# Kernel optimization log

Hardware: AMD Instinct MI355X
Metric: run time of the kernel (lower is better)

Reference implementation:

```python
import jax, jax.numpy as jnp
import numpy as np

T = 4096          # prefill tokens (single sequence)
HK = 16           # key heads
HV = 32           # value heads
DK = 128          # key head dim
DV = 128          # value head dim
K = 4             # causal conv kernel width
QKV = 2 * HK * DK + HV * DV  # 8192


def setup_inputs() -> dict:
    key = jax.random.key(0)
    k1, k2, k3, k4, k5, k6 = jax.random.split(key, 6)
    return {
        "mixed_qkv": jax.random.normal(k1, (T, QKV), dtype=jnp.float32),
        "a": jax.random.normal(k2, (T, HV), dtype=jnp.float32),
        "b": jax.random.normal(k3, (T, HV), dtype=jnp.float32),
        "conv_w": jax.random.normal(k4, (QKV, K), dtype=jnp.float32) * 0.2,
        "dt_bias": jax.random.normal(k5, (HV,), dtype=jnp.float32),
        "alog": jax.random.normal(k6, (HV,), dtype=jnp.float32),
    }


def _l2norm(x, eps=1e-6):
    return x * jax.lax.rsqrt(jnp.sum(x * x, axis=-1, keepdims=True) + eps)


def _forward(mixed_qkv, a, b, conv_w, dt_bias, alog):
    # --- causal depthwise conv1d (zero initial conv state) + SiLU ---
    xp = jnp.pad(mixed_qkv, ((K - 1, 0), (0, 0)))  # [T+K-1, QKV]
    y = sum(conv_w[None, :, j] * xp[j:j + T] for j in range(K))  # [T, QKV]
    x = jax.nn.silu(y)

    # --- split q/k/v ---
    q, k_, v = jnp.split(x, [HK * DK, 2 * HK * DK], axis=-1)
    q = q.reshape(T, HK, DK)
    k_ = k_.reshape(T, HK, DK)
    v = v.reshape(T, HV, DV)

    # use_qk_l2norm_in_kernel=True: L2-norm q,k; scale q by dk^-0.5
    q = _l2norm(q) * (DK ** -0.5)
    k_ = _l2norm(k_)

    # GQA: repeat key-head q/k to value-head count
    grp = HV // HK
    q = jnp.repeat(q, grp, axis=1)   # [T, HV, DK]
    k_ = jnp.repeat(k_, grp, axis=1)  # [T, HV, DK]

    # --- fused_gdn_gating ---
    g = -jnp.exp(alog)[None, :] * jax.nn.softplus(a + dt_bias[None, :])  # [T, HV]
    beta = jax.nn.sigmoid(b)                                             # [T, HV]

    # --- gated delta-rule recurrence (equiv. to chunk_gated_delta_rule) ---
    S0 = jnp.zeros((HV, DK, DV), dtype=mixed_qkv.dtype)

    def step(S, inp):
        qt, kt, vt, gt, bt = inp
        S = S * jnp.exp(gt)[:, None, None]                 # gated decay
        pred = jnp.einsum('hk,hkv->hv', kt, S)             # k^T S
        delta = (vt - pred) * bt[:, None]                  # beta-scaled error
        S = S + jnp.einsum('hk,hv->hkv', kt, delta)        # delta update
        o = jnp.einsum('hk,hkv->hv', qt, S)                # query readout
        return S, o

    _, out = jax.lax.scan(step, S0, (q, k_, v, g, beta))
    return out  # [T, HV, DV]


def reference(mixed_qkv, a, b, conv_w, dt_bias, alog):
    return _forward(mixed_qkv, a, b, conv_w, dt_bias, alog)
```

## Files before the change

kernel.cpp:

```cpp
#include <hip/hip_runtime.h>

#define T_LEN 4096
#define HKn   16
#define HVn   32
#define DKn   128
#define DVn   128
#define QKVn  8192
#define NCH   64
#define CS    64

typedef __attribute__((ext_vector_type(8))) short short8;
typedef __attribute__((ext_vector_type(4))) float f32x4;
typedef __attribute__((ext_vector_type(4))) unsigned u32x4;

#define OFF_QSH  ((size_t)0)
#define OFF_QSL  ((size_t)16777216)
#define OFF_KSH  ((size_t)33554432)
#define OFF_KSL  ((size_t)50331648)
#define OFF_KTH  ((size_t)67108864)
#define OFF_KTL  ((size_t)83886080)
#define OFF_VA   ((size_t)100663296)
#define OFF_GBL  ((size_t)167772160)
#define OFF_G    ((size_t)168820736)
#define OFF_WH   ((size_t)169345024)
#define OFF_WL   ((size_t)202899456)
#define OFF_MH   ((size_t)236453888)
#define OFF_ML   ((size_t)253231104)

template <int CTRL>
__device__ __forceinline__ float dpp_add(float x) {
    int v = __builtin_amdgcn_update_dpp(0, __float_as_int(x), CTRL, 0xF, 0xF, true);
    return x + __int_as_float(v);
}
__device__ __forceinline__ float reduce32g(float x) {
    x = dpp_add<0x128>(x); x = dpp_add<0x124>(x);
    x = dpp_add<0x122>(x); x = dpp_add<0x121>(x);
    int v = __builtin_amdgcn_ds_swizzle(__float_as_int(x), 0x401F);
    return x + __int_as_float(v);
}
__device__ __forceinline__ unsigned short bf16rne(float f) {
    unsigned x = __float_as_uint(f);
    return (unsigned short)((x + 0x7FFFu + ((x >> 16) & 1u)) >> 16);
}
__device__ __forceinline__ float bf16tof(unsigned short h) {
    return __uint_as_float(((unsigned)h) << 16);
}
__device__ __forceinline__ void bsplit(float f, unsigned short& h, unsigned short& l) {
    h = bf16rne(f);
    l = bf16rne(f - bf16tof(h));
}
__device__ __forceinline__ unsigned packsplit(float f) {
    unsigned short h, l; bsplit(f, h, l);
    return ((unsigned)h << 16) | (unsigned)l;
}
__device__ __forceinline__ f32x4 MF(short8 a, short8 b, f32x4 c) {
    return __builtin_amdgcn_mfma_f32_16x16x32_bf16(a, b, c, 0, 0, 0);
}
__device__ __forceinline__ void unpack8(u32x4 x0, u32x4 x1, short8& hi, short8& lo) {
    union { u32x4 u; short8 s; } H, L;
    H.u[0] = __builtin_amdgcn_perm(x0.y, x0.x, 0x07060302u);
    L.u[0] = __builtin_amdgcn_perm(x0.y, x0.x, 0x05040100u);
    H.u[1] = __builtin_amdgcn_perm(x0.w, x0.z, 0x07060302u);
    L.u[1] = __builtin_amdgcn_perm(x0.w, x0.z, 0x05040100u);
    H.u[2] = __builtin_amdgcn_perm(x1.y, x1.x, 0x07060302u);
    L.u[2] = __builtin_amdgcn_perm(x1.y, x1.x, 0x05040100u);
    H.u[3] = __builtin_amdgcn_perm(x1.w, x1.z, 0x07060302u);
    L.u[3] = __builtin_amdgcn_perm(x1.w, x1.z, 0x05040100u);
    hi = H.s; lo = L.s;
}
#define SB0() __builtin_amdgcn_sched_barrier(0)
#define BARL() do { \
    asm volatile("s_waitcnt lgkmcnt(0)" ::: "memory"); \
    __builtin_amdgcn_s_barrier(); \
    asm volatile("" ::: "memory"); \
} while (0)

__global__ __launch_bounds__(256) void k_gate(
    const float* __restrict__ a, const float* __restrict__ b,
    const float* __restrict__ dt_bias, const float* __restrict__ alog,
    float2* __restrict__ gbl)
{
    const int i = blockIdx.x * 256 + threadIdx.x;
    if (i < T_LEN * HVn) {
        const int h = i >> 12, t = i & (T_LEN - 1);
        const float av = a[(size_t)t * HVn + h];
        const float bv = b[(size_t)t * HVn + h];
        const float xv = av + dt_bias[h];
        const float sp = fmaxf(xv, 0.f) + log1pf(expf(-fabsf(xv)));
        const float g  = -expf(alog[h]) * sp;
        const float beta = 1.f / (1.f + expf(-bv));
        gbl[(size_t)h * T_LEN + t] = make_float2(beta, g);
    }
}

__global__ __launch_bounds__(128) void k_conv(
    const float* __restrict__ x, const float* __restrict__ w,
    const float* __restrict__ bgate,
    unsigned short* __restrict__ qsh, unsigned short* __restrict__ qsl,
    unsigned short* __restrict__ ksh, unsigned short* __restrict__ ksl,
    float* __restrict__ va2)
{
    const int t = blockIdx.x, seg = blockIdx.y, d = threadIdx.x;
    const int c = seg * 128 + d;
    const float4 w4 = ((const float4*)w)[c];
    float acc;
    if (t >= 3) {
        const float* xc = x + (size_t)(t - 3) * QKVn + c;
        acc = fmaf(w4.x, xc[0], fmaf(w4.y, xc[(size_t)QKVn],
              fmaf(w4.z, xc[(size_t)2 * QKVn], w4.w * xc[(size_t)3 * QKVn])));
    } else {
        float a0 = (t - 3 >= 0) ? x[(size_t)(t - 3) * QKVn + c] : 0.f;
        float a1 = (t - 2 >= 0) ? x[(size_t)(t - 2) * QKVn + c] : 0.f;
        float a2 = (t - 1 >= 0) ? x[(size_t)(t - 1) * QKVn + c] : 0.f;
        float a3 = x[(size_t)t * QKVn + c];
        acc = fmaf(w4.x, a0, fmaf(w4.y, a1, fmaf(w4.z, a2, w4.w * a3)));
    }
    const float y = acc / (1.f + expf(-acc));

    if (seg < 32) {
        float ss = reduce32g(y * y);
        __shared__ float part[4];
        if ((threadIdx.x & 31) == 0) part[threadIdx.x >> 5] = ss;
        __syncthreads();
        const float total = part[0] + part[1] + part[2] + part[3];
        const float r = rsqrtf(total + 1e-6f);
        float o = y * r;
        unsigned short hh, ll;
        if (seg < 16) {
            o *= 0.08838834764831845f;
            bsplit(o, hh, ll);
            const size_t idx = ((size_t)seg * T_LEN + t) * DKn + d;
            qsh[idx] = hh; qsl[idx] = ll;
        } else {
            bsplit(o, hh, ll);
            const size_t idx = ((size_t)(seg - 16) * T_LEN + t) * DKn + d;
            ksh[idx] = hh; ksl[idx] = ll;
        }
    } else {
        const int h = seg - 32;
        const float bv = bgate[(size_t)t * HVn + h];
        const float beta = 1.f / (1.f + expf(-bv));
        va2[((size_t)h * T_LEN + t) * DVn + d] = y * beta;
    }
}

__global__ __launch_bounds__(256) void k_tr(
    const unsigned short* __restrict__ ksh, const unsigned short* __restrict__ ksl,
    unsigned short* __restrict__ kth, unsigned short* __restrict__ ktl)
{
    __shared__ unsigned pk[64][65];
    const int b = blockIdx.x;
    const int kh = b >> 7, tt = (b >> 1) & 63, hh = b & 1;
    const int t0 = tt * 64, d0 = hh * 64;
    const int tid = threadIdx.x;
    #pragma unroll
    for (int e = 0; e < 16; ++e) {
        const int lin = e * 256 + tid;
        const int tl = lin >> 6, dl = lin & 63;
        const size_t o = ((size_t)kh * T_LEN + t0 + tl) * DKn + d0 + dl;
        pk[tl][dl] = ((unsigned)ksh[o] << 16) | (unsigned)ksl[o];
    }
    __syncthreads();
    #pragma unroll
    for (int e = 0; e < 16; ++e) {
        const int lin = e * 256 + tid;
        const int dl = lin >> 6, tl = lin & 63;
        const unsigned v = pk[tl][dl];
        const size_t o = ((size_t)kh * DKn + d0 + dl) * T_LEN + t0 + tl;
        kth[o] = (unsigned short)(v >> 16);
        ktl[o] = (unsigned short)(v & 0xFFFF);
    }
}

__global__ __launch_bounds__(256) void k_p1(
    const float2* __restrict__ gbl,
    const unsigned short* __restrict__ qsh, const unsigned short* __restrict__ qsl,
    const unsigned short* __restrict__ ksh, const unsigned short* __restrict__ ksl,
    float* __restrict__ va2, float* __restrict__ Gbuf,
    unsigned short* __restrict__ Wh, unsigned short* __restrict__ Wl,
    unsigned short* __restrict__ Mh, unsigned short* __restrict__ Ml)
{
    __shared__ float sA[64][68];
    __shared__ float sG[64];
    __shared__ float sB[64];
    const int blk = blockIdx.x;
    const int h = blk >> 6, ch = blk & 63;
    const int kh = h >> 1, t0 = ch * 64;
    const int tid = threadIdx.x, lane = tid & 63, wid = tid >> 6;
    const int l15 = lane & 15, lg = lane >> 4;

    if (tid < 64) {
        float2 g2 = gbl[(size_t)h * T_LEN + t0 + tid];
        sB[tid] = g2.x;
        float G = g2.y;
        #pragma unroll
        for (int s = 1; s < 64; s <<= 1) {
            float y = __int_as_float(__builtin_amdgcn_ds_bpermute((tid - s) << 2, __float_as_int(G)));
            G += (tid >= s) ? y : 0.f;
        }
        sG[tid] = G;
        Gbuf[(size_t)h * T_LEN + t0 + tid] = G;
    }
    __syncthreads();

    const char TIa[10] = {0,1,1,2,2,2,3,3,3,3};
    const char TJa[10] = {0,0,1,0,1,2,0,1,2,3};
    const size_t kbase = ((size_t)kh * T_LEN + t0) * DKn;
    for (int idx = wid; idx < 10; idx += 4) {
        const int mi = TIa[idx], nj = TJa[idx];
        f32x4 aKK = {0.f,0.f,0.f,0.f}, aQK = {0.f,0.f,0.f,0.f};
        #pragma unroll
        for (int kk = 0; kk < 4; ++kk) {
            const size_t offA = kbase + (size_t)(16*mi + l15) * DKn + 32*kk + 8*lg;
            const size_t offB = kbase + (size_t)(16*nj + l15) * DKn + 32*kk + 8*lg;
            short8 kAh = *(const short8*)(ksh + offA);
            short8 kAl = *(const short8*)(ksl + offA);
            short8 kBh = *(const short8*)(ksh + offB);
            short8 kBl = *(const short8*)(ksl + offB);
            short8 qAh = *(const short8*)(qsh + offA);
            short8 qAl = *(const short8*)(qsl + offA);
            aKK = MF(kAh,kBh,aKK); aKK = MF(kAh,kBl,aKK); aKK = MF(kAl,kBh,aKK);
            aQK = MF(qAh,kBh,aQK); aQK = MF(qAh,kBl,aQK); aQK = MF(qAl,kBh,aQK);
        }
        #pragma unroll
        for (int r = 0; r < 4; ++r) {
            const int i = 16*mi + 4*lg + r;
            const int j = 16*nj + l15;
            const float e = __expf(fminf(sG[i] - sG[j], 0.f));
            sA[i][j] = (j < i) ? sB[i] * e * aKK[r] : 0.f;
            const float mv = (j <= i) ? e * aQK[r] : 0.f;
            unsigned short mh, ml; bsplit(mv, mh, ml);
            const size_t moff = (((size_t)h * NCH + ch) * CS + i) * CS + j;
            Mh[moff] = mh; Ml[moff] = ml;
        }
    }
    __syncthreads();

    const int c = tid;
    float X[64];
    if (c < 128) {
        #pragma unroll
        for (int i = 0; i < 64; ++i)
            X[i] = va2[((size_t)h * T_LEN + t0 + i) * DVn + c];
    } else {
        const int dk = c - 128;
        #pragma unroll
        for (int i = 0; i < 64; ++i) {
            const size_t o = ((size_t)kh * T_LEN + t0 + i) * DKn + dk;
            const float kf = bf16tof(ksh[o]) + bf16tof(ksl[o]);
            X[i] = sB[i] * __expf(sG[i]) * kf;
        }
    }
    #pragma unroll
    for (int i = 1; i < 64; ++i) {
        float acc = X[i];
        const int nq = (i + 3) >> 2;
        #pragma unroll
        for (int q = 0; q < nq; ++q) {
            const f32x4 aa = *(const f32x4*)&sA[i][4*q];
            acc = fmaf(-aa[0], X[4*q+0], acc);
            acc = fmaf(-aa[1], X[4*q+1], acc);
            acc = fmaf(-aa[2], X[4*q+2], acc);
            acc = fmaf(-aa[3], X[4*q+3], acc);
        }
        X[i] = acc;
    }
    if (c < 128) {
        #pragma unroll
        for (int i = 0; i < 64; ++i)
            va2[((size_t)h * T_LEN + t0 + i) * DVn + c] = X[i];
    } else {
        const int dk = c - 128;
        #pragma unroll
        for (int i = 0; i < 64; ++i) {
            unsigned short wh, wl; bsplit(-X[i], wh, wl);
            const size_t o = (((size_t)h * NCH + ch) * CS + i) * DKn + dk;
            Wh[o] = wh; Wl[o] = wl;
        }
    }
}

struct ChBuf {
    short8 qh[4], ql[4];
    short8 wh[4], wl[4];
    short8 mh[2], ml[2];
    short8 th[2][2], tl[2][2];
    float  u[4];
    float4 g4;
    float  g63;
};

__device__ __forceinline__ void issue_ch(ChBuf& B, int ch,
    const unsigned short* __restrict__ qsh, const unsigned short* __restrict__ qsl,
    const unsigned short* __restrict__ kth, const unsigned short* __restrict__ ktl,
    const unsigned short* __restrict__ Wh, const unsigned short* __restrict__ Wl,
    const unsigned short* __restrict__ Mh, const unsigned short* __restrict__ Ml,
    const float* __restrict__ va2, const float* __restrict__ Gbuf,
    int h, int kh, int n0, int wid, int l15, int lg)
{
    const int t0 = ch * CS;
    const size_t qbase = ((size_t)kh * T_LEN + t0 + 16*wid + l15) * DKn;
    #pragma unroll
    for (int kk = 0; kk < 4; ++kk) {
        B.qh[kk] = *(const short8*)(qsh + qbase + 32*kk + 8*lg);
        B.ql[kk] = *(const short8*)(qsl + qbase + 32*kk + 8*lg);
    }
    const size_t wbase = (((size_t)h * NCH + ch) * CS + 16*wid + l15) * DKn;
    #pragma unroll
    for (int kk = 0; kk < 4; ++kk) {
        B.wh[kk] = *(const short8*)(Wh + wbase + 32*kk + 8*lg);
        B.wl[kk] = *(const short8*)(Wl + wbase + 32*kk + 8*lg);
    }
    const size_t mbase = (((size_t)h * NCH + ch) * CS + 16*wid + l15) * CS;
    #pragma unroll
    for (int k2 = 0; k2 < 2; ++k2) {
        B.mh[k2] = *(const short8*)(Mh + mbase + 32*k2 + 8*lg);
        B.ml[k2] = *(const short8*)(Ml + mbase + 32*k2 + 8*lg);
    }
    #pragma unroll
    for (int m2 = 0; m2 < 2; ++m2) {
        const size_t kb2 = ((size_t)kh * DKn + 16*(wid + 4*m2) + l15) * T_LEN + t0;
        #pragma unroll
        for (int k2 = 0; k2 < 2; ++k2) {
            B.th[m2][k2] = *(const short8*)(kth + kb2 + 32*k2 + 8*lg);
            B.tl[m2][k2] = *(const short8*)(ktl + kb2 + 32*k2 + 8*lg);
        }
    }
    #pragma unroll
    for (int r = 0; r < 4; ++r)
        B.u[r] = va2[((size_t)h * T_LEN + t0 + 16*wid + 4*lg + r) * DVn + n0 + l15];
    const float* gp = Gbuf + (size_t)h * T_LEN + t0;
    B.g4  = *(const float4*)(gp + 16*wid + 4*lg);
    B.g63 = gp[63];
}

__device__ __forceinline__ void compute_ch(const ChBuf& B, int ch,
    unsigned (*sSp)[132], unsigned (*sDLp)[68], unsigned (*sDSp)[68],
    short8* Sbh, short8* Sbl, f32x4* Sc,
    float* __restrict__ out,
    int h, int n0, int wid, int l15, int lg)
{
    const int t0 = ch * CS;
    const float g63 = B.g63;
    const float gr[4] = {B.g4.x, B.g4.y, B.g4.z, B.g4.w};

    f32x4 dl;
    #pragma unroll
    for (int r = 0; r < 4; ++r) dl[r] = B.u[r];
    #pragma unroll
    for (int kk = 0; kk < 4; ++kk) {
        dl = MF(B.wh[kk], Sbh[kk], dl); dl = MF(B.wh[kk], Sbl[kk], dl); dl = MF(B.wl[kk], Sbh[kk], dl);
    }

    const int cc0 = 16*wid + 4*lg;
    u32x4 pdl, pds;
    #pragma unroll
    for (int r = 0; r < 4; ++r) {
        pdl[r] = packsplit(dl[r]);
        pds[r] = packsplit(dl[r] * __expf(g63 - gr[r]));
    }
    *(u32x4*)&sDLp[l15][cc0] = pdl;
    *(u32x4*)&sDSp[l15][cc0] = pds;
    BARL();

    short8 dlh[2], dll[2], dsh[2], dsl[2];
    #pragma unroll
    for (int k2 = 0; k2 < 2; ++k2) {
        u32x4 x0 = *(const u32x4*)&sDLp[l15][32*k2 + 8*lg];
        u32x4 x1 = *(const u32x4*)&sDLp[l15][32*k2 + 8*lg + 4];
        unpack8(x0, x1, dlh[k2], dll[k2]);
        u32x4 y0 = *(const u32x4*)&sDSp[l15][32*k2 + 8*lg];
        u32x4 y1 = *(const u32x4*)&sDSp[l15][32*k2 + 8*lg + 4];
        unpack8(y0, y1, dsh[k2], dsl[k2]);
    }

    f32x4 aq = {0.f,0.f,0.f,0.f}, am = {0.f,0.f,0.f,0.f};
    #pragma unroll
    for (int kk = 0; kk < 4; ++kk) {
        aq = MF(B.qh[kk], Sbh[kk], aq); aq = MF(B.qh[kk], Sbl[kk], aq); aq = MF(B.ql[kk], Sbh[kk], aq);
    }
    #pragma unroll
    for (int k2 = 0; k2 < 2; ++k2) {
        am = MF(B.mh[k2], dlh[k2], am); am = MF(B.mh[k2], dll[k2], am); am = MF(B.ml[k2], dlh[k2], am);
    }
    #pragma unroll
    for (int r = 0; r < 4; ++r) {
        const int cc = cc0 + r;
        out[((size_t)(t0 + cc) * HVn + h) * DVn + n0 + l15] = fmaf(__expf(gr[r]), aq[r], am[r]);
    }

    const float lam = __expf(g63);
    #pragma unroll
    for (int m2 = 0; m2 < 2; ++m2) {
        f32x4 t4 = {0.f,0.f,0.f,0.f};
        #pragma unroll
        for (int k2 = 0; k2 < 2; ++k2) {
            t4 = MF(B.th[m2][k2], dsh[k2], t4); t4 = MF(B.th[m2][k2], dsl[k2], t4); t4 = MF(B.tl[m2][k2], dsh[k2], t4);
        }
        u32x4 ps;
        #pragma unroll
        for (int r = 0; r < 4; ++r) {
            Sc[m2][r] = fmaf(lam, Sc[m2][r], t4[r]);
            ps[r] = packsplit(Sc[m2][r]);
        }
        *(u32x4*)&sSp[l15][16*wid + 64*m2 + 4*lg] = ps;
    }
    BARL();

    #pragma unroll
    for (int kk = 0; kk < 4; ++kk) {
        u32x4 z0 = *(const u32x4*)&sSp[l15][32*kk + 8*lg];
        u32x4 z1 = *(const u32x4*)&sSp[l15][32*kk + 8*lg + 4];
        unpack8(z0, z1, Sbh[kk], Sbl[kk]);
    }
}

__global__ __launch_bounds__(256, 1) void k_p2(
    const unsigned short* __restrict__ qsh, const unsigned short* __restrict__ qsl,
    const unsigned short* __restrict__ kth, const unsigned short* __restrict__ ktl,
    const unsigned short* __restrict__ Wh, const unsigned short* __restrict__ Wl,
    const unsigned short* __restrict__ Mh, const unsigned short* __restrict__ Ml,
    const float* __restrict__ va2, const float* __restrict__ Gbuf,
    float* __restrict__ out)
{
    __shared__ unsigned sSp[16][132];
    __shared__ unsigned sDLp[16][68];
    __shared__ unsigned sDSp[16][68];

    const int p = blockIdx.x;
    const int slot = p >> 3;
    const int h  = (p & 7) * 4 + (slot & 3);
    const int nb = slot >> 2;
    const int kh = h >> 1, n0 = nb * 16;
    const int tid = threadIdx.x, lane = tid & 63, wid = tid >> 6;
    const int l15 = lane & 15, lg = lane >> 4;

    short8 Sbh[4], Sbl[4];
    f32x4 Sc[2];
    const short8 z8 = {0,0,0,0,0,0,0,0};
    #pragma unroll
    for (int kk = 0; kk < 4; ++kk) { Sbh[kk] = z8; Sbl[kk] = z8; }
    Sc[0] = (f32x4){0.f,0.f,0.f,0.f};
    Sc[1] = (f32x4){0.f,0.f,0.f,0.f};

    ChBuf bufA, bufB;
    issue_ch(bufA, 0, qsh, qsl, kth, ktl, Wh, Wl, Mh, Ml, va2, Gbuf,
             h, kh, n0, wid, l15, lg);

    #pragma unroll 1
    for (int ch2 = 0; ch2 < NCH / 2; ++ch2) {
        const int ch = 2 * ch2;
        SB0();
        issue_ch(bufB, ch + 1, qsh, qsl, kth, ktl, Wh, Wl, Mh, Ml, va2, Gbuf,
                 h, kh, n0, wid, l15, lg);
        SB0();
        compute_ch(bufA, ch, sSp, sDLp, sDSp, Sbh, Sbl, Sc, out, h, n0, wid, l15, lg);
        SB0();
        if (ch + 2 < NCH)
            issue_ch(bufA, ch + 2, qsh, qsl, kth, ktl, Wh, Wl, Mh, Ml, va2, Gbuf,
                     h, kh, n0, wid, l15, lg);
        SB0();
        compute_ch(bufB, ch + 1, sSp, sDLp, sDSp, Sbh, Sbl, Sc, out, h, n0, wid, l15, lg);
    }
}

extern "C" void kernel_launch(void* const* d_in, const int* in_sizes, int n_in,
                              void* d_out, int out_size, void* d_ws, size_t ws_size,
                              hipStream_t stream) {
    const float* mixed_qkv = (const float*)d_in[0];
    const float* a         = (const float*)d_in[1];
    const float* b         = (const float*)d_in[2];
    const float* conv_w    = (const float*)d_in[3];
    const float* dt_bias   = (const float*)d_in[4];
    const float* alog      = (const float*)d_in[5];
    float* out = (float*)d_out;
    char* ws = (char*)d_ws;

    unsigned short* qsh = (unsigned short*)(ws + OFF_QSH);
    unsigned short* qsl = (unsigned short*)(ws + OFF_QSL);
    unsigned short* ksh = (unsigned short*)(ws + OFF_KSH);
    unsigned short* ksl = (unsigned short*)(ws + OFF_KSL);
    unsigned short* kth = (unsigned short*)(ws + OFF_KTH);
    unsigned short* ktl = (unsigned short*)(ws + OFF_KTL);
    float*  va2 = (float*)(ws + OFF_VA);
    float2* gbl = (float2*)(ws + OFF_GBL);
    float*  Gbf = (float*)(ws + OFF_G);
    unsigned short* Wh = (unsigned short*)(ws + OFF_WH);
    unsigned short* Wl = (unsigned short*)(ws + OFF_WL);
    unsigned short* Mh = (unsigned short*)(ws + OFF_MH);
    unsigned short* Ml = (unsigned short*)(ws + OFF_ML);

    k_gate<<<(T_LEN * HVn + 255) / 256, 256, 0, stream>>>(a, b, dt_bias, alog, gbl);

    dim3 cgrid(T_LEN, 64);
    k_conv<<<cgrid, 128, 0, stream>>>(mixed_qkv, conv_w, b, qsh, qsl, ksh, ksl, va2);

    k_tr<<<2048, 256, 0, stream>>>(ksh, ksl, kth, ktl);

    k_p1<<<HVn * NCH, 256, 0, stream>>>(gbl, qsh, qsl, ksh, ksl, va2, Gbf, Wh, Wl, Mh, Ml);

    k_p2<<<HVn * 8, 256, 0, stream>>>(qsh, qsl, kth, ktl, Wh, Wl, Mh, Ml, va2, Gbf, out);
}
```

Measured before the change: 528.0 us.

## Stage per-chunk operands through LDS with direct global-to-LDS loads

Replaces the register double-buffered chunk prefetch (two ChBuf structs) in the recurrence kernel with per-wave LDS staging filled by global_load_lds instructions. MFMA operands are then read from LDS inside the compute step, and each chunk's loads are issued at the end of the previous iteration. The aim is to free the many VGPRs held by the two register buffers and to cut load-issue overhead. In exchange there is a single buffer, and an immediate vmcnt(0) wait at the top of each iteration, which also covers the output stores, so load latency is largely exposed rather than overlapped. It also adds extra LDS reads on the critical path.

```diff
diff --git a/kernel.cpp b/kernel.cpp
--- a/kernel.cpp
+++ b/kernel.cpp
@@ -74,6 +74,23 @@
     __builtin_amdgcn_s_barrier(); \
     asm volatile("" ::: "memory"); \
 } while (0)
+#define WAITV0() do { \
+    asm volatile("s_waitcnt vmcnt(0)" ::: "memory"); \
+    SB0(); \
+} while (0)
+#define WAITL0() do { \
+    asm volatile("s_waitcnt lgkmcnt(0)" ::: "memory"); \
+    SB0(); \
+} while (0)
+
+typedef __attribute__((address_space(3))) void lds_t;
+typedef const __attribute__((address_space(1))) void gbl_t;
+__device__ __forceinline__ void load_lds16(const void* g, void* l) {
+    __builtin_amdgcn_global_load_lds((gbl_t*)g, (lds_t*)l, 16, 0, 0);
+}
+__device__ __forceinline__ void load_lds4(const void* g, void* l) {
+    __builtin_amdgcn_global_load_lds((gbl_t*)g, (lds_t*)l, 4, 0, 0);
+}
 
 __global__ __launch_bounds__(256) void k_gate(
     const float* __restrict__ a, const float* __restrict__ b,
@@ -280,140 +297,10 @@
     }
 }
 
-struct ChBuf {
-    short8 qh[4], ql[4];
-    short8 wh[4], wl[4];
-    short8 mh[2], ml[2];
-    short8 th[2][2], tl[2][2];
-    float  u[4];
-    float4 g4;
-    float  g63;
-};
-
-__device__ __forceinline__ void issue_ch(ChBuf& B, int ch,
-    const unsigned short* __restrict__ qsh, const unsigned short* __restrict__ qsl,
-    const unsigned short* __restrict__ kth, const unsigned short* __restrict__ ktl,
-    const unsigned short* __restrict__ Wh, const unsigned short* __restrict__ Wl,
-    const unsigned short* __restrict__ Mh, const unsigned short* __restrict__ Ml,
-    const float* __restrict__ va2, const float* __restrict__ Gbuf,
-    int h, int kh, int n0, int wid, int l15, int lg)
-{
-    const int t0 = ch * CS;
-    const size_t qbase = ((size_t)kh * T_LEN + t0 + 16*wid + l15) * DKn;
-    #pragma unroll
-    for (int kk = 0; kk < 4; ++kk) {
-        B.qh[kk] = *(const short8*)(qsh + qbase + 32*kk + 8*lg);
-        B.ql[kk] = *(const short8*)(qsl + qbase + 32*kk + 8*lg);
-    }
-    const size_t wbase = (((size_t)h * NCH + ch) * CS + 16*wid + l15) * DKn;
-    #pragma unroll
-    for (int kk = 0; kk < 4; ++kk) {
-        B.wh[kk] = *(const short8*)(Wh + wbase + 32*kk + 8*lg);
-        B.wl[kk] = *(const short8*)(Wl + wbase + 32*kk + 8*lg);
-    }
-    const size_t mbase = (((size_t)h * NCH + ch) * CS + 16*wid + l15) * CS;
-    #pragma unroll
-    for (int k2 = 0; k2 < 2; ++k2) {
-        B.mh[k2] = *(const short8*)(Mh + mbase + 32*k2 + 8*lg);
-        B.ml[k2] = *(const short8*)(Ml + mbase + 32*k2 + 8*lg);
-    }
-    #pragma unroll
-    for (int m2 = 0; m2 < 2; ++m2) {
-        const size_t kb2 = ((size_t)kh * DKn + 16*(wid + 4*m2) + l15) * T_LEN + t0;
-        #pragma unroll
-        for (int k2 = 0; k2 < 2; ++k2) {
-            B.th[m2][k2] = *(const short8*)(kth + kb2 + 32*k2 + 8*lg);
-            B.tl[m2][k2] = *(const short8*)(ktl + kb2 + 32*k2 + 8*lg);
-        }
-    }
-    #pragma unroll
-    for (int r = 0; r < 4; ++r)
-        B.u[r] = va2[((size_t)h * T_LEN + t0 + 16*wid + 4*lg + r) * DVn + n0 + l15];
-    const float* gp = Gbuf + (size_t)h * T_LEN + t0;
-    B.g4  = *(const float4*)(gp + 16*wid + 4*lg);
-    B.g63 = gp[63];
-}
-
-__device__ __forceinline__ void compute_ch(const ChBuf& B, int ch,
-    unsigned (*sSp)[132], unsigned (*sDLp)[68], unsigned (*sDSp)[68],
-    short8* Sbh, short8* Sbl, f32x4* Sc,
-    float* __restrict__ out,
-    int h, int n0, int wid, int l15, int lg)
-{
-    const int t0 = ch * CS;
-    const float g63 = B.g63;
-    const float gr[4] = {B.g4.x, B.g4.y, B.g4.z, B.g4.w};
-
-    f32x4 dl;
-    #pragma unroll
-    for (int r = 0; r < 4; ++r) dl[r] = B.u[r];
-    #pragma unroll
-    for (int kk = 0; kk < 4; ++kk) {
-        dl = MF(B.wh[kk], Sbh[kk], dl); dl = MF(B.wh[kk], Sbl[kk], dl); dl = MF(B.wl[kk], Sbh[kk], dl);
-    }
-
-    const int cc0 = 16*wid + 4*lg;
-    u32x4 pdl, pds;
-    #pragma unroll
-    for (int r = 0; r < 4; ++r) {
-        pdl[r] = packsplit(dl[r]);
-        pds[r] = packsplit(dl[r] * __expf(g63 - gr[r]));
-    }
-    *(u32x4*)&sDLp[l15][cc0] = pdl;
-    *(u32x4*)&sDSp[l15][cc0] = pds;
-    BARL();
-
-    short8 dlh[2], dll[2], dsh[2], dsl[2];
-    #pragma unroll
-    for (int k2 = 0; k2 < 2; ++k2) {
-        u32x4 x0 = *(const u32x4*)&sDLp[l15][32*k2 + 8*lg];
-        u32x4 x1 = *(const u32x4*)&sDLp[l15][32*k2 + 8*lg + 4];
-        unpack8(x0, x1, dlh[k2], dll[k2]);
-        u32x4 y0 = *(const u32x4*)&sDSp[l15][32*k2 + 8*lg];
-        u32x4 y1 = *(const u32x4*)&sDSp[l15][32*k2 + 8*lg + 4];
-        unpack8(y0, y1, dsh[k2], dsl[k2]);
-    }
-
-    f32x4 aq = {0.f,0.f,0.f,0.f}, am = {0.f,0.f,0.f,0.f};
-    #pragma unroll
-    for (int kk = 0; kk < 4; ++kk) {
-        aq = MF(B.qh[kk], Sbh[kk], aq); aq = MF(B.qh[kk], Sbl[kk], aq); aq = MF(B.ql[kk], Sbh[kk], aq);
-    }
-    #pragma unroll
-    for (int k2 = 0; k2 < 2; ++k2) {
-        am = MF(B.mh[k2], dlh[k2], am); am = MF(B.mh[k2], dll[k2], am); am = MF(B.ml[k2], dlh[k2], am);
-    }
-    #pragma unroll
-    for (int r = 0; r < 4; ++r) {
-        const int cc = cc0 + r;
-        out[((size_t)(t0 + cc) * HVn + h) * DVn + n0 + l15] = fmaf(__expf(gr[r]), aq[r], am[r]);
-    }
-
-    const float lam = __expf(g63);
-    #pragma unroll
-    for (int m2 = 0; m2 < 2; ++m2) {
-        f32x4 t4 = {0.f,0.f,0.f,0.f};
-        #pragma unroll
-        for (int k2 = 0; k2 < 2; ++k2) {
-            t4 = MF(B.th[m2][k2], dsh[k2], t4); t4 = MF(B.th[m2][k2], dsl[k2], t4); t4 = MF(B.tl[m2][k2], dsh[k2], t4);
-        }
-        u32x4 ps;
-        #pragma unroll
-        for (int r = 0; r < 4; ++r) {
-            Sc[m2][r] = fmaf(lam, Sc[m2][r], t4[r]);
-            ps[r] = packsplit(Sc[m2][r]);
-        }
-        *(u32x4*)&sSp[l15][16*wid + 64*m2 + 4*lg] = ps;
-    }
-    BARL();
-
-    #pragma unroll
-    for (int kk = 0; kk < 4; ++kk) {
-        u32x4 z0 = *(const u32x4*)&sSp[l15][32*kk + 8*lg];
-        u32x4 z1 = *(const u32x4*)&sSp[l15][32*kk + 8*lg + 4];
-        unpack8(z0, z1, Sbh[kk], Sbl[kk]);
-    }
-}
+#define SLOT  1024
+#define OFF_GROW 28672
+#define OFF_U    28928
+#define WSTG  29952
 
 __global__ __launch_bounds__(256, 1) void k_p2(
     const unsigned short* __restrict__ qsh, const unsigned short* __restrict__ qsl,
@@ -423,6 +310,7 @@
     const float* __restrict__ va2, const float* __restrict__ Gbuf,
     float* __restrict__ out)
 {
+    __shared__ __align__(16) char stg[4][WSTG];
     __shared__ unsigned sSp[16][132];
     __shared__ unsigned sDLp[16][68];
     __shared__ unsigned sDSp[16][68];
@@ -435,6 +323,8 @@
     const int tid = threadIdx.x, lane = tid & 63, wid = tid >> 6;
     const int l15 = lane & 15, lg = lane >> 4;
 
+    char* wb = &stg[wid][0];
+
     short8 Sbh[4], Sbl[4];
     f32x4 Sc[2];
     const short8 z8 = {0,0,0,0,0,0,0,0};
@@ -443,24 +333,141 @@
     Sc[0] = (f32x4){0.f,0.f,0.f,0.f};
     Sc[1] = (f32x4){0.f,0.f,0.f,0.f};
 
-    ChBuf bufA, bufB;
-    issue_ch(bufA, 0, qsh, qsl, kth, ktl, Wh, Wl, Mh, Ml, va2, Gbuf,
-             h, kh, n0, wid, l15, lg);
+    auto stage_ch = [&](int ch) {
+        const int t0 = ch * CS;
+        const size_t wbase = (((size_t)h * NCH + ch) * CS + 16*wid + l15) * DKn + 8*lg;
+        #pragma unroll
+        for (int kk = 0; kk < 4; ++kk) {
+            load_lds16(Wh + wbase + 32*kk, wb + (0 + kk) * SLOT);
+            load_lds16(Wl + wbase + 32*kk, wb + (4 + kk) * SLOT);
+        }
+        const size_t kb0 = ((size_t)kh * DKn + 16*wid + l15) * T_LEN + t0 + 8*lg;
+        const size_t kb1 = ((size_t)kh * DKn + 16*(wid + 4) + l15) * T_LEN + t0 + 8*lg;
+        #pragma unroll
+        for (int k2 = 0; k2 < 2; ++k2) {
+            load_lds16(kth + kb0 + 32*k2, wb + (8  + k2) * SLOT);
+            load_lds16(kth + kb1 + 32*k2, wb + (10 + k2) * SLOT);
+            load_lds16(ktl + kb0 + 32*k2, wb + (12 + k2) * SLOT);
+            load_lds16(ktl + kb1 + 32*k2, wb + (14 + k2) * SLOT);
+        }
+        const size_t qbase = ((size_t)kh * T_LEN + t0 + 16*wid + l15) * DKn + 8*lg;
+        #pragma unroll
+        for (int kk = 0; kk < 4; ++kk) {
+            load_lds16(qsh + qbase + 32*kk, wb + (16 + kk) * SLOT);
+            load_lds16(qsl + qbase + 32*kk, wb + (20 + kk) * SLOT);
+        }
+        const size_t mbase = (((size_t)h * NCH + ch) * CS + 16*wid + l15) * CS + 8*lg;
+        #pragma unroll
+        for (int k2 = 0; k2 < 2; ++k2) {
+            load_lds16(Mh + mbase + 32*k2, wb + (24 + k2) * SLOT);
+            load_lds16(Ml + mbase + 32*k2, wb + (26 + k2) * SLOT);
+        }
+        load_lds4(Gbuf + (size_t)h * T_LEN + t0 + lane, wb + OFF_GROW);
+        #pragma unroll
+        for (int r = 0; r < 4; ++r)
+            load_lds4(va2 + ((size_t)h * T_LEN + t0 + 16*wid + 4*lg + r) * DVn + n0 + l15,
+                      wb + OFF_U + r * 256);
+    };
+
+    stage_ch(0);
 
     #pragma unroll 1
-    for (int ch2 = 0; ch2 < NCH / 2; ++ch2) {
-        const int ch = 2 * ch2;
-        SB0();
-        issue_ch(bufB, ch + 1, qsh, qsl, kth, ktl, Wh, Wl, Mh, Ml, va2, Gbuf,
-                 h, kh, n0, wid, l15, lg);
-        SB0();
-        compute_ch(bufA, ch, sSp, sDLp, sDSp, Sbh, Sbl, Sc, out, h, n0, wid, l15, lg);
-        SB0();
-        if (ch + 2 < NCH)
-            issue_ch(bufA, ch + 2, qsh, qsl, kth, ktl, Wh, Wl, Mh, Ml, va2, Gbuf,
-                     h, kh, n0, wid, l15, lg);
-        SB0();
-        compute_ch(bufB, ch + 1, sSp, sDLp, sDSp, Sbh, Sbl, Sc, out, h, n0, wid, l15, lg);
+    for (int ch = 0; ch < NCH; ++ch) {
+        const int t0 = ch * CS;
+        WAITV0();
+
+        const float* gw = (const float*)(wb + OFF_GROW);
+        float gr[4];
+        #pragma unroll
+        for (int r = 0; r < 4; ++r) gr[r] = gw[16*wid + 4*lg + r];
+        const float g63 = gw[63];
+        const float lam = __expf(g63);
+        float scE[4], eg[4];
+        #pragma unroll
+        for (int r = 0; r < 4; ++r) { scE[r] = __expf(g63 - gr[r]); eg[r] = __expf(gr[r]); }
+        float uf[4];
+        #pragma unroll
+        for (int r = 0; r < 4; ++r) uf[r] = *(const float*)(wb + OFF_U + r * 256 + lane * 4);
+
+        f32x4 dl = {uf[0], uf[1], uf[2], uf[3]};
+        #pragma unroll
+        for (int kk = 0; kk < 4; ++kk) {
+            const short8 wh8 = *(const short8*)(wb + (0 + kk) * SLOT + lane * 16);
+            const short8 wl8 = *(const short8*)(wb + (4 + kk) * SLOT + lane * 16);
+            dl = MF(wh8, Sbh[kk], dl); dl = MF(wh8, Sbl[kk], dl); dl = MF(wl8, Sbh[kk], dl);
+        }
+
+        const int cc0 = 16*wid + 4*lg;
+        u32x4 pdl, pds;
+        #pragma unroll
+        for (int r = 0; r < 4; ++r) {
+            pdl[r] = packsplit(dl[r]);
+            pds[r] = packsplit(dl[r] * scE[r]);
+        }
+        *(u32x4*)&sDLp[l15][cc0] = pdl;
+        *(u32x4*)&sDSp[l15][cc0] = pds;
+        BARL();
+
+        short8 dlh[2], dll[2], dsh[2], dsl[2];
+        #pragma unroll
+        for (int k2 = 0; k2 < 2; ++k2) {
+            u32x4 x0 = *(const u32x4*)&sDLp[l15][32*k2 + 8*lg];
+            u32x4 x1 = *(const u32x4*)&sDLp[l15][32*k2 + 8*lg + 4];
+            unpack8(x0, x1, dlh[k2], dll[k2]);
+            u32x4 y0 = *(const u32x4*)&sDSp[l15][32*k2 + 8*lg];
+            u32x4 y1 = *(const u32x4*)&sDSp[l15][32*k2 + 8*lg + 4];
+            unpack8(y0, y1, dsh[k2], dsl[k2]);
+        }
+
+        f32x4 aq = {0.f,0.f,0.f,0.f}, am = {0.f,0.f,0.f,0.f};
+        #pragma unroll
+        for (int kk = 0; kk < 4; ++kk) {
+            const short8 qh8 = *(const short8*)(wb + (16 + kk) * SLOT + lane * 16);
+            const short8 ql8 = *(const short8*)(wb + (20 + kk) * SLOT + lane * 16);
+            aq = MF(qh8, Sbh[kk], aq); aq = MF(qh8, Sbl[kk], aq); aq = MF(ql8, Sbh[kk], aq);
+        }
+        #pragma unroll
+        for (int k2 = 0; k2 < 2; ++k2) {
+            const short8 mh8 = *(const short8*)(wb + (24 + k2) * SLOT + lane * 16);
+            const short8 ml8 = *(const short8*)(wb + (26 + k2) * SLOT + lane * 16);
+            am = MF(mh8, dlh[k2], am); am = MF(mh8, dll[k2], am); am = MF(ml8, dlh[k2], am);
+        }
+        #pragma unroll
+        for (int r = 0; r < 4; ++r) {
+            const int cc = cc0 + r;
+            out[((size_t)(t0 + cc) * HVn + h) * DVn + n0 + l15] = fmaf(eg[r], aq[r], am[r]);
+        }
+
+        #pragma unroll
+        for (int m2 = 0; m2 < 2; ++m2) {
+            f32x4 t4 = {0.f,0.f,0.f,0.f};
+            #pragma unroll
+            for (int k2 = 0; k2 < 2; ++k2) {
+                const short8 th8 = *(const short8*)(wb + (8 + 2*m2 + k2) * SLOT + lane * 16);
+                const short8 tl8 = *(const short8*)(wb + (12 + 2*m2 + k2) * SLOT + lane * 16);
+                t4 = MF(th8, dsh[k2], t4); t4 = MF(th8, dsl[k2], t4); t4 = MF(tl8, dsh[k2], t4);
+            }
+            u32x4 ps;
+            #pragma unroll
+            for (int r = 0; r < 4; ++r) {
+                Sc[m2][r] = fmaf(lam, Sc[m2][r], t4[r]);
+                ps[r] = packsplit(Sc[m2][r]);
+            }
+            *(u32x4*)&sSp[l15][16*wid + 64*m2 + 4*lg] = ps;
+        }
+        BARL();
+
+        #pragma unroll
+        for (int kk = 0; kk < 4; ++kk) {
+            u32x4 z0 = *(const u32x4*)&sSp[l15][32*kk + 8*lg];
+            u32x4 z1 = *(const u32x4*)&sSp[l15][32*kk + 8*lg + 4];
+            unpack8(z0, z1, Sbh[kk], Sbl[kk]);
+        }
+
+        if (ch + 1 < NCH) {
+            WAITL0();
+            stage_ch(ch + 1);
+        }
     }
 }
 
```

New measurement: 581.2 us. +10.1%, slower.
